# Kernel optimization log

Measured on AMD Instinct MI355X. Metric: run time of the kernel, lower is better.

## Reference

```python
import jax, jax.numpy as jnp
import numpy as np

D_MODEL = 1024
NUM_HEADS = 16
HEAD_DIM = D_MODEL // NUM_HEADS
B, S = 2, 2048


def setup_inputs() -> dict:
    key = jax.random.key(0)
    ks = jax.random.split(key, 10)
    sc = 1.0 / np.sqrt(D_MODEL)
    return {
        "x": jax.random.normal(ks[0], (B, S, D_MODEL), jnp.float32),
        "y": jax.random.normal(ks[1], (B, S, D_MODEL), jnp.float32),
        "Wkv": jax.random.normal(ks[2], (D_MODEL, 2 * D_MODEL), jnp.float32) * sc,
        "bkv": jax.random.normal(ks[3], (2 * D_MODEL,), jnp.float32) * 0.01,
        "Wq": jax.random.normal(ks[4], (D_MODEL, D_MODEL), jnp.float32) * sc,
        "bq": jax.random.normal(ks[5], (D_MODEL,), jnp.float32) * 0.01,
        "Wo": jax.random.normal(ks[6], (D_MODEL, D_MODEL), jnp.float32) * sc,
        "bo": jax.random.normal(ks[7], (D_MODEL,), jnp.float32) * 0.01,
    }


def reference(x, y, Wkv, bkv, Wq, bq, Wo, bo):
    b, s, d = x.shape
    # projections: kv from x (keys/values come from encoder side), q from y
    kv = x @ Wkv + bkv                      # [B, S, 2*d_model]
    q = y @ Wq + bq                         # [B, S, d_model]
    kv = kv.reshape(b, s, NUM_HEADS, 2 * HEAD_DIM).transpose(0, 2, 1, 3)  # [B,H,S,2*hd]
    q = q.reshape(b, s, NUM_HEADS, HEAD_DIM).transpose(0, 2, 1, 3)        # [B,H,S,hd]
    k, v = jnp.split(kv, 2, axis=-1)        # each [B,H,S,hd]
    scaled = jnp.einsum("bhqd,bhkd->bhqk", q, k) / np.sqrt(HEAD_DIM)      # [B,H,S,S]
    attention = jax.nn.softmax(scaled, axis=-1)
    values = jnp.einsum("bhqk,bhkd->bhqd", attention, v)                  # [B,H,S,hd]
    values = values.transpose(0, 2, 1, 3).reshape(b, s, d)                # [B,S,d_model]
    return values @ Wo + bo
```

## Files before the change

### kernel.cpp

```cpp
#include <hip/hip_runtime.h>
#include <hip/hip_bf16.h>

typedef __attribute__((ext_vector_type(8))) short short8;
typedef __attribute__((ext_vector_type(4))) short short4v;
typedef __attribute__((ext_vector_type(4))) float f32x4;
typedef __attribute__((ext_vector_type(16))) float f32x16;

#define B_  2
#define S_  2048
#define H_  16
#define HD_ 64
#define D_  1024
#define QSCALE 0.18033688f

__device__ __forceinline__ short f2bs(float f) {
  union { float f; unsigned u; } c; c.f = f;
  unsigned u = c.u;
  u += 0x7fffu + ((u >> 16) & 1u);
  return (short)(u >> 16);
}

__device__ __forceinline__ unsigned pack_bf16(float a, float b) {
  __hip_bfloat162 h = __float22bfloat162_rn(float2{a, b});
  return *reinterpret_cast<unsigned*>(&h);
}

__device__ __forceinline__ float fexp2(float x) {
#if __has_builtin(__builtin_amdgcn_exp2f)
  return __builtin_amdgcn_exp2f(x);
#else
  return exp2f(x);
#endif
}

__device__ __forceinline__ float frcp(float x) {
#if __has_builtin(__builtin_amdgcn_rcpf)
  return __builtin_amdgcn_rcpf(x);
#else
  return 1.0f / x;
#endif
}

#define GL2LDS(gp, lp) __builtin_amdgcn_global_load_lds( \
    (const __attribute__((address_space(1))) unsigned int*)(gp), \
    (__attribute__((address_space(3))) unsigned int*)(lp), 16, 0, 0)

#define WAITCNT4  asm volatile("s_waitcnt vmcnt(4)" ::: "memory")
#define WAITCNT8  asm volatile("s_waitcnt vmcnt(8)" ::: "memory")
#define WAITCNT0  asm volatile("s_waitcnt vmcnt(0)" ::: "memory")
#define BARRIER_PIN do { __builtin_amdgcn_s_barrier(); __builtin_amdgcn_sched_barrier(0); } while (0)

__global__ __launch_bounds__(256)
void prep_kernel(const float* __restrict__ x, const float* __restrict__ y,
                 short* __restrict__ xb, short* __restrict__ yb,
                 const float* __restrict__ Wkv, short* __restrict__ Wkvt,
                 const float* __restrict__ Wq, short* __restrict__ Wqt,
                 const float* __restrict__ Wo, short* __restrict__ Wot) {
  __shared__ float tile[64][65];
  int bx = blockIdx.x;
  if (bx < 8192) {
    int i = bx * 256 + threadIdx.x;
    const float4* src; short4v* dst; int j;
    if (i < (1 << 20)) { src = (const float4*)x; dst = (short4v*)xb; j = i; }
    else               { src = (const float4*)y; dst = (short4v*)yb; j = i - (1 << 20); }
    float4 f = src[j];
    short4v o;
    o.x = f2bs(f.x); o.y = f2bs(f.y); o.z = f2bs(f.z); o.w = f2bs(f.w);
    dst[j] = o;
    return;
  }
  bx -= 8192;
  const float* in; short* out; int C, c0, r0;
  if (bx < 512)      { in = Wkv; out = Wkvt; C = 2048; c0 = (bx & 31) * 64; r0 = (bx >> 5) * 64; }
  else if (bx < 768) { bx -= 512; in = Wq; out = Wqt; C = 1024; c0 = (bx & 15) * 64; r0 = (bx >> 4) * 64; }
  else               { bx -= 768; in = Wo; out = Wot; C = 1024; c0 = (bx & 15) * 64; r0 = (bx >> 4) * 64; }
  const int tx = threadIdx.x & 63, ty = threadIdx.x >> 6;
#pragma unroll
  for (int i = 0; i < 16; ++i) {
    int r = ty + i * 4;
    tile[r][tx] = in[(size_t)(r0 + r) * C + c0 + tx];
  }
  __syncthreads();
#pragma unroll
  for (int i = 0; i < 16; ++i) {
    int r = ty + i * 4;
    out[(size_t)(c0 + r) * 1024 + r0 + tx] = f2bs(tile[tx][r]);
  }
}

template <int MODE>
__device__ __forceinline__ void gemm_body(const short* __restrict__ A, const short* __restrict__ Bt,
                                          const float* __restrict__ bias,
                                          void* __restrict__ out0, void* __restrict__ out1,
                                          int m0, int n0, int K, short* smem) {
  short* As_ = smem;
  short* Bs_ = smem + 12288;
  const int tid = threadIdx.x;
  const int w = tid >> 6, lane = tid & 63;
  const int q15 = lane & 15, quad = lane >> 4;
  const int wm = (w >> 1) * 64, wn = (w & 1) * 64;

  f32x4 acc[4][4];
#pragma unroll
  for (int i = 0; i < 4; ++i)
#pragma unroll
    for (int j = 0; j < 4; ++j) acc[i][j] = f32x4{0.f, 0.f, 0.f, 0.f};

  const int srow = w * 16 + (lane >> 2);
  const int gch  = (lane & 3) ^ ((lane >> 3) & 3);
  const short* Ag = A + (size_t)(m0 + srow) * K + gch * 8;
  const short* Bg = Bt + (size_t)(n0 + srow) * K + gch * 8;
  const int lof = srow * 32 + (lane & 3) * 8;

#define STAGE_AB(t, buf) do { \
    const short* a2 = Ag + (size_t)(t) * 32; \
    const short* b2 = Bg + (size_t)(t) * 32; \
    short* ad = As_ + (buf) * 4096 + lof; \
    short* bd = Bs_ + (buf) * 4096 + lof; \
    GL2LDS(a2,                  ad); \
    GL2LDS(a2 + (size_t)64 * K, ad + 2048); \
    GL2LDS(b2,                  bd); \
    GL2LDS(b2 + (size_t)64 * K, bd + 2048); \
  } while (0)

  const int NT = K >> 5;
  STAGE_AB(0, 0);
  STAGE_AB(1, 1);
  int cb = 0, ib = 2;
  for (int kt = 0; kt < NT; ++kt) {
    if (kt < NT - 1) WAITCNT4; else WAITCNT0;
    BARRIER_PIN;
    if (kt + 2 < NT) STAGE_AB(kt + 2, ib);
    const short* Ac = As_ + cb * 4096;
    const short* Bc = Bs_ + cb * 4096;
    short8 af[4], bf[4];
#pragma unroll
    for (int mi = 0; mi < 4; ++mi) {
      int rr = wm + mi * 16 + q15;
      af[mi] = *(const short8*)(Ac + rr * 32 + ((quad ^ ((rr >> 1) & 3)) * 8));
    }
#pragma unroll
    for (int ni = 0; ni < 4; ++ni) {
      int rr = wn + ni * 16 + q15;
      bf[ni] = *(const short8*)(Bc + rr * 32 + ((quad ^ ((rr >> 1) & 3)) * 8));
    }
#pragma unroll
    for (int mi = 0; mi < 4; ++mi)
#pragma unroll
      for (int ni = 0; ni < 4; ++ni)
        acc[mi][ni] = __builtin_amdgcn_mfma_f32_16x16x32_bf16(af[mi], bf[ni], acc[mi][ni], 0, 0, 0);
    cb = (cb == 2) ? 0 : cb + 1;
    ib = (ib == 2) ? 0 : ib + 1;
  }
#undef STAGE_AB
  __syncthreads();

  if constexpr (MODE == 0) {
#pragma unroll
    for (int mi = 0; mi < 4; ++mi)
#pragma unroll
      for (int ni = 0; ni < 4; ++ni) {
        const int n = n0 + wn + ni * 16 + q15;
        const float bn = bias[n];
#pragma unroll
        for (int r = 0; r < 4; ++r) {
          const int m = m0 + wm + mi * 16 + quad * 4 + r;
          int b = m >> 11, s = m & 2047, hh = n >> 6, d = n & 63;
          ((short*)out0)[((size_t)((b * H_ + hh) * S_ + s) << 6) + d] = f2bs((acc[mi][ni][r] + bn) * QSCALE);
        }
      }
  } else {
    const int hh = n0 >> 7;
    const int bb = m0 >> 11;
    const size_t bh = (size_t)(bb * H_ + hh);
    const int s0 = m0 & 2047;
    if ((w & 1) == 0) {
#pragma unroll
      for (int mi = 0; mi < 4; ++mi)
#pragma unroll
        for (int ni = 0; ni < 4; ++ni) {
          const float bn = bias[n0 + ni * 16 + q15];
#pragma unroll
          for (int r = 0; r < 4; ++r) {
            const int s = s0 + wm + mi * 16 + quad * 4 + r;
            ((short*)out0)[((bh * S_ + s) << 6) + ni * 16 + q15] = f2bs(acc[mi][ni][r] + bn);
          }
        }
    } else {
      short* VT = smem;
#pragma unroll
      for (int mi = 0; mi < 4; ++mi)
#pragma unroll
        for (int ni = 0; ni < 4; ++ni) {
          const int d = ni * 16 + q15;
          const float bn = bias[n0 + 64 + ni * 16 + q15];
#pragma unroll
          for (int t = 0; t < 2; ++t) {
            const int chunk = (wm >> 1) + mi * 8 + quad * 2 + t;
            unsigned pk = pack_bf16(acc[mi][ni][2 * t] + bn, acc[mi][ni][2 * t + 1] + bn);
            *reinterpret_cast<unsigned*>(VT + d * 128 + ((chunk ^ (d & 15)) * 2)) = pk;
          }
        }
    }
    __syncthreads();
    {
      short* VT = smem;
      const int d = tid >> 2, t4 = tid & 3;
      unsigned vals[16];
#pragma unroll
      for (int c = 0; c < 16; ++c) {
        int chunk = t4 * 16 + c;
        vals[c] = *reinterpret_cast<unsigned*>(VT + d * 128 + ((chunk ^ (d & 15)) * 2));
      }
      uint4* dst = (uint4*)((short*)out1 + ((bh * HD_ + d) << 11) + s0 + t4 * 32);
      dst[0] = uint4{vals[0], vals[1], vals[4],  vals[5]};
      dst[1] = uint4{vals[2], vals[3], vals[6],  vals[7]};
      dst[2] = uint4{vals[8], vals[9], vals[12], vals[13]};
      dst[3] = uint4{vals[10], vals[11], vals[14], vals[15]};
    }
  }
}

__global__ __launch_bounds__(256)
void proj_kernel(const short* __restrict__ xb, const short* __restrict__ Wkvt,
                 const float* __restrict__ bkv, short* __restrict__ Kb, short* __restrict__ Vtb,
                 const short* __restrict__ yb, const short* __restrict__ Wqt,
                 const float* __restrict__ bq, short* __restrict__ Qb) {
  __shared__ __align__(16) short smem[24576];
  int bx = blockIdx.x;
  bx = (bx & 7) * 96 + (bx >> 3);
  if (bx < 512)
    gemm_body<1>(xb, Wkvt, bkv, Kb, Vtb, (bx >> 4) * 128, (bx & 15) * 128, 1024, smem);
  else {
    bx -= 512;
    gemm_body<0>(yb, Wqt, bq, Qb, nullptr, (bx >> 3) * 128, (bx & 7) * 128, 1024, smem);
  }
}

__global__ __launch_bounds__(256)
void gemm_o_kernel(const short* __restrict__ A, const short* __restrict__ Bt,
                   const float* __restrict__ bias, float* __restrict__ out) {
  __shared__ __align__(16) short lds[16384];
  const int tid = threadIdx.x;
  const int w = tid >> 6, lane = tid & 63;
  const int q15 = lane & 15, quad = lane >> 4;
  const int m0 = blockIdx.y * 64, n0 = blockIdx.x * 64;
  const int wm = (w >> 1) * 32, wn = (w & 1) * 32;
  const int xw = q15 & 7;

  f32x4 acc[2][2];
#pragma unroll
  for (int i = 0; i < 2; ++i)
#pragma unroll
    for (int j = 0; j < 2; ++j) acc[i][j] = f32x4{0.f, 0.f, 0.f, 0.f};

  const int srow = w * 8 + (lane >> 3);
  const int gch  = (lane & 7) ^ (srow & 7);
  const int loff = w * 512 + lane * 8;
  const short* Ag = A + (size_t)(m0 + srow) * 1024 + gch * 8;
  const short* Bg = Bt + (size_t)(n0 + srow) * 1024 + gch * 8;

  GL2LDS(Ag,             lds + loff);
  GL2LDS(Ag + 32 * 1024, lds + loff + 2048);
  GL2LDS(Bg,             lds + 8192 + loff);
  GL2LDS(Bg + 32 * 1024, lds + 8192 + loff + 2048);

  for (int kt = 0; kt < 16; ++kt) {
    __syncthreads();
    const short* Ac = lds + ((kt & 1) ? 4096 : 0);
    const short* Bc = lds + 8192 + ((kt & 1) ? 4096 : 0);
    if (kt < 15) {
      const short* a2 = Ag + (kt + 1) * 64;
      const short* b2 = Bg + (kt + 1) * 64;
      short* ad = lds + ((kt & 1) ? 0 : 4096) + loff;
      short* bd = lds + 8192 + ((kt & 1) ? 0 : 4096) + loff;
      GL2LDS(a2,             ad);
      GL2LDS(a2 + 32 * 1024, ad + 2048);
      GL2LDS(b2,             bd);
      GL2LDS(b2 + 32 * 1024, bd + 2048);
    }
    short8 af[2][2], bf[2][2];
#pragma unroll
    for (int mi = 0; mi < 2; ++mi)
#pragma unroll
      for (int kk = 0; kk < 2; ++kk)
        af[mi][kk] = *(const short8*)(Ac + (wm + mi * 16 + q15) * 64 + (((kk * 4 + quad) ^ xw) * 8));
#pragma unroll
    for (int ni = 0; ni < 2; ++ni)
#pragma unroll
      for (int kk = 0; kk < 2; ++kk)
        bf[ni][kk] = *(const short8*)(Bc + (wn + ni * 16 + q15) * 64 + (((kk * 4 + quad) ^ xw) * 8));
#pragma unroll
    for (int mi = 0; mi < 2; ++mi)
#pragma unroll
      for (int ni = 0; ni < 2; ++ni)
#pragma unroll
        for (int kk = 0; kk < 2; ++kk)
          acc[mi][ni] = __builtin_amdgcn_mfma_f32_16x16x32_bf16(af[mi][kk], bf[ni][kk], acc[mi][ni], 0, 0, 0);
  }

#pragma unroll
  for (int mi = 0; mi < 2; ++mi)
#pragma unroll
    for (int ni = 0; ni < 2; ++ni) {
      const int n = n0 + wn + ni * 16 + q15;
      const float bn = bias[n];
#pragma unroll
      for (int r = 0; r < 4; ++r) {
        const int m = m0 + wm + mi * 16 + quad * 4 + r;
        out[(size_t)m * 1024 + n] = acc[mi][ni][r] + bn;
      }
    }
}

__global__ __launch_bounds__(256, 2)
void attn_kernel(const short* __restrict__ Q, const short* __restrict__ K,
                 const short* __restrict__ Vt, short* __restrict__ Out) {
  __shared__ __align__(16) short lds[32768];
  short* QP = lds + 24576;
  const int tid = threadIdx.x;
  const int w = tid >> 6, lane = tid & 63;
  const int l31 = lane & 31, h5 = lane >> 5;
  const int rsw = l31 & 7;
  const int bx = blockIdx.x;
  const int xcd = bx & 7, slot = bx >> 3;
  const int pp = xcd * 4 + (slot >> 4);
  const int qt = slot & 15;
  const int h = pp & 15, b = pp >> 4;
  const size_t bh = (size_t)(b * H_ + h);
  const short* Qg = Q + bh * (S_ * HD_) + qt * (128 * HD_);
  const short* Kg = K + bh * (S_ * HD_);
  const short* Vg = Vt + bh * (HD_ * S_);

  const int srow = tid >> 3;
  const int gch  = (tid & 7) ^ (srow & 7);
  const int loff = tid * 8;

  const short* kg = Kg + srow * 64 + gch * 8;
  const short* vg = Vg + (size_t)srow * S_ + gch * 8;

#define STAGE_KV(t, buf) do { \
    const short* k2 = kg + (size_t)(t) * 4096; \
    const short* v2 = vg + (size_t)(t) * 64; \
    short* kd = lds + (buf) * 4096 + loff; \
    short* vd = lds + 12288 + (buf) * 4096 + loff; \
    GL2LDS(k2,                   kd); \
    GL2LDS(k2 + 2048,            kd + 2048); \
    GL2LDS(v2,                   vd); \
    GL2LDS(v2 + (size_t)32 * S_, vd + 2048); \
  } while (0)

  {
    const short* qg = Qg + srow * 64 + gch * 8;
#pragma unroll
    for (int t = 0; t < 4; ++t) GL2LDS(qg + t * 2048, QP + loff + t * 2048);
  }
  STAGE_KV(0, 0);
  STAGE_KV(1, 1);
  WAITCNT8;
  BARRIER_PIN;

  short8 aq[4];
#pragma unroll
  for (int kk = 0; kk < 4; ++kk)
    aq[kk] = *(const short8*)(QP + (w * 32 + l31) * 64 + (((kk * 2 + h5) ^ rsw) * 8));

  f32x16 oacc[2];
#pragma unroll
  for (int i = 0; i < 16; ++i) { oacc[0][i] = 0.f; oacc[1][i] = 0.f; }
  float lsum = 0.f;
  f32x16 z16;
#pragma unroll
  for (int i = 0; i < 16; ++i) z16[i] = 0.f;

  int cb = 0, ib = 2;
  for (int kt = 0; kt < 32; ++kt) {
    if (kt < 31) WAITCNT4; else WAITCNT0;
    BARRIER_PIN;
    if (kt + 2 < 32) STAGE_KV(kt + 2, ib);
    const short* Kc = lds + cb * 4096;
    const short* Vc = lds + 12288 + cb * 4096;

    f32x16 sacc[2];
    __builtin_amdgcn_s_setprio(1);
#pragma unroll
    for (int sb = 0; sb < 2; ++sb) {
      const short* kr = Kc + (sb * 32 + l31) * 64;
      short8 k0 = *(const short8*)(kr + (((0 + h5) ^ rsw) * 8));
      short8 k1 = *(const short8*)(kr + (((2 + h5) ^ rsw) * 8));
      short8 k2 = *(const short8*)(kr + (((4 + h5) ^ rsw) * 8));
      short8 k3 = *(const short8*)(kr + (((6 + h5) ^ rsw) * 8));
      f32x16 s = __builtin_amdgcn_mfma_f32_32x32x16_bf16(k0, aq[0], z16, 0, 0, 0);
      s = __builtin_amdgcn_mfma_f32_32x32x16_bf16(k1, aq[1], s, 0, 0, 0);
      s = __builtin_amdgcn_mfma_f32_32x32x16_bf16(k2, aq[2], s, 0, 0, 0);
      s = __builtin_amdgcn_mfma_f32_32x32x16_bf16(k3, aq[3], s, 0, 0, 0);
      sacc[sb] = s;
    }
    __builtin_amdgcn_s_setprio(0);

    short8 ap[4];
#pragma unroll
    for (int sb = 0; sb < 2; ++sb) {
      float e[16];
#pragma unroll
      for (int i = 0; i < 16; ++i) e[i] = fexp2(sacc[sb][i]);
      lsum += (((e[0] + e[1]) + (e[2] + e[3])) + ((e[4] + e[5]) + (e[6] + e[7])))
            + (((e[8] + e[9]) + (e[10] + e[11])) + ((e[12] + e[13]) + (e[14] + e[15])));
      union { unsigned u[4]; short8 s8; } lo, hi;
      lo.u[0] = pack_bf16(e[0], e[1]);   lo.u[1] = pack_bf16(e[2], e[3]);
      lo.u[2] = pack_bf16(e[4], e[5]);   lo.u[3] = pack_bf16(e[6], e[7]);
      hi.u[0] = pack_bf16(e[8], e[9]);   hi.u[1] = pack_bf16(e[10], e[11]);
      hi.u[2] = pack_bf16(e[12], e[13]); hi.u[3] = pack_bf16(e[14], e[15]);
      ap[sb * 2 + 0] = lo.s8;
      ap[sb * 2 + 1] = hi.s8;
    }

    __builtin_amdgcn_s_setprio(1);
#pragma unroll
    for (int db = 0; db < 2; ++db) {
      const short* vr = Vc + (db * 32 + l31) * 64;
      short8 v0 = *(const short8*)(vr + (((0 + h5) ^ rsw) * 8));
      short8 v1 = *(const short8*)(vr + (((2 + h5) ^ rsw) * 8));
      short8 v2 = *(const short8*)(vr + (((4 + h5) ^ rsw) * 8));
      short8 v3 = *(const short8*)(vr + (((6 + h5) ^ rsw) * 8));
      f32x16 o = oacc[db];
      o = __builtin_amdgcn_mfma_f32_32x32x16_bf16(ap[0], v0, o, 0, 0, 0);
      o = __builtin_amdgcn_mfma_f32_32x32x16_bf16(ap[1], v1, o, 0, 0, 0);
      o = __builtin_amdgcn_mfma_f32_32x32x16_bf16(ap[2], v2, o, 0, 0, 0);
      o = __builtin_amdgcn_mfma_f32_32x32x16_bf16(ap[3], v3, o, 0, 0, 0);
      oacc[db] = o;
    }
    __builtin_amdgcn_s_setprio(0);
    cb = (cb == 2) ? 0 : cb + 1;
    ib = (ib == 2) ? 0 : ib + 1;
  }
#undef STAGE_KV

  float lt = lsum + __shfl_xor(lsum, 32);
  float inv[16];
#pragma unroll
  for (int r = 0; r < 16; ++r)
    inv[r] = frcp(__shfl(lt, (r & 3) + 8 * (r >> 2) + 4 * h5, 64));
#pragma unroll
  for (int db = 0; db < 2; ++db) {
    const int col = h * HD_ + db * 32 + l31;
#pragma unroll
    for (int r = 0; r < 16; ++r) {
      const int m = b * S_ + qt * 128 + w * 32 + (r & 3) + 8 * (r >> 2) + 4 * h5;
      Out[(size_t)m * D_ + col] = f2bs(oacc[db][r] * inv[r]);
    }
  }
}

extern "C" void kernel_launch(void* const* d_in, const int* in_sizes, int n_in,
                              void* d_out, int out_size, void* d_ws, size_t ws_size,
                              hipStream_t stream) {
  const float* x   = (const float*)d_in[0];
  const float* y   = (const float*)d_in[1];
  const float* Wkv = (const float*)d_in[2];
  const float* bkv = (const float*)d_in[3];
  const float* Wq  = (const float*)d_in[4];
  const float* bq  = (const float*)d_in[5];
  const float* Wo  = (const float*)d_in[6];
  const float* bo  = (const float*)d_in[7];
  float* out = (float*)d_out;

  short* xb   = (short*)d_ws;
  short* yb   = xb + (4 << 20);
  short* Wkvt = yb + (4 << 20);
  short* Wqt  = Wkvt + (2 << 20);
  short* Wot  = Wqt + (1 << 20);
  short* Kb   = Wot + (1 << 20);
  short* Vtb  = Kb + (4 << 20);
  short* Qb   = Vtb + (4 << 20);
  short* AOb  = Qb + (4 << 20);

  prep_kernel<<<9216, 256, 0, stream>>>(x, y, xb, yb, Wkv, Wkvt, Wq, Wqt, Wo, Wot);
  proj_kernel<<<768, 256, 0, stream>>>(xb, Wkvt, bkv, Kb, Vtb, yb, Wqt, bq, Qb);
  attn_kernel<<<512, 256, 0, stream>>>(Qb, Kb, Vtb, AOb);
  gemm_o_kernel<<<dim3(16, 64), 256, 0, stream>>>(AOb, Wot, bo, out);
}
```

Baseline: 192.8 us.

## Software-pipeline attention loop: overlap QK of tile t with PV of tile t-1

Restructures the attention inner loop so each step computes QK^T for the current K tile and PV for the previous tile's probabilities, with the softmax/exp of the current tile done after the MFMAs. The goal is to let exp and pack work overlap with matrix-core work instead of serialising QK, softmax and PV within one tile. V tiles get a fourth LDS buffer (LDS grows from 64KB to 72KB) because V lives one step longer. This adds a prologue and epilogue, doubles the registers held for probabilities, and the larger LDS footprint may affect occupancy at two blocks per CU.

```diff
diff --git a/kernel.cpp b/kernel.cpp
--- a/kernel.cpp
+++ b/kernel.cpp
@@ -46,7 +46,6 @@
     (__attribute__((address_space(3))) unsigned int*)(lp), 16, 0, 0)
 
 #define WAITCNT4  asm volatile("s_waitcnt vmcnt(4)" ::: "memory")
-#define WAITCNT8  asm volatile("s_waitcnt vmcnt(8)" ::: "memory")
 #define WAITCNT0  asm volatile("s_waitcnt vmcnt(0)" ::: "memory")
 #define BARRIER_PIN do { __builtin_amdgcn_s_barrier(); __builtin_amdgcn_sched_barrier(0); } while (0)
 
@@ -316,8 +315,8 @@
 __global__ __launch_bounds__(256, 2)
 void attn_kernel(const short* __restrict__ Q, const short* __restrict__ K,
                  const short* __restrict__ Vt, short* __restrict__ Out) {
-  __shared__ __align__(16) short lds[32768];
-  short* QP = lds + 24576;
+  __shared__ __align__(16) short lds[36864];
+  short* QP = lds + 28672;
   const int tid = threadIdx.x;
   const int w = tid >> 6, lane = tid & 63;
   const int l31 = lane & 31, h5 = lane >> 5;
@@ -339,25 +338,102 @@
   const short* kg = Kg + srow * 64 + gch * 8;
   const short* vg = Vg + (size_t)srow * S_ + gch * 8;
 
-#define STAGE_KV(t, buf) do { \
+#define STAGE_KV(t, kb, vb) do { \
     const short* k2 = kg + (size_t)(t) * 4096; \
     const short* v2 = vg + (size_t)(t) * 64; \
-    short* kd = lds + (buf) * 4096 + loff; \
-    short* vd = lds + 12288 + (buf) * 4096 + loff; \
+    short* kd = lds + (kb) * 4096 + loff; \
+    short* vd = lds + 12288 + (vb) * 4096 + loff; \
     GL2LDS(k2,                   kd); \
     GL2LDS(k2 + 2048,            kd + 2048); \
     GL2LDS(v2,                   vd); \
     GL2LDS(v2 + (size_t)32 * S_, vd + 2048); \
   } while (0)
 
+#define QK_CLUSTER(Kc, S0, S1) do { \
+    const short* kr0 = (Kc) + l31 * 64; \
+    const short* kr1 = (Kc) + (32 + l31) * 64; \
+    short8 k0 = *(const short8*)(kr0 + (((0 + h5) ^ rsw) * 8)); \
+    short8 k1 = *(const short8*)(kr0 + (((2 + h5) ^ rsw) * 8)); \
+    short8 k2 = *(const short8*)(kr0 + (((4 + h5) ^ rsw) * 8)); \
+    short8 k3 = *(const short8*)(kr0 + (((6 + h5) ^ rsw) * 8)); \
+    short8 m0 = *(const short8*)(kr1 + (((0 + h5) ^ rsw) * 8)); \
+    short8 m1 = *(const short8*)(kr1 + (((2 + h5) ^ rsw) * 8)); \
+    short8 m2 = *(const short8*)(kr1 + (((4 + h5) ^ rsw) * 8)); \
+    short8 m3 = *(const short8*)(kr1 + (((6 + h5) ^ rsw) * 8)); \
+    S0 = __builtin_amdgcn_mfma_f32_32x32x16_bf16(k0, aq[0], z16, 0, 0, 0); \
+    S0 = __builtin_amdgcn_mfma_f32_32x32x16_bf16(k1, aq[1], S0, 0, 0, 0); \
+    S0 = __builtin_amdgcn_mfma_f32_32x32x16_bf16(k2, aq[2], S0, 0, 0, 0); \
+    S0 = __builtin_amdgcn_mfma_f32_32x32x16_bf16(k3, aq[3], S0, 0, 0, 0); \
+    S1 = __builtin_amdgcn_mfma_f32_32x32x16_bf16(m0, aq[0], z16, 0, 0, 0); \
+    S1 = __builtin_amdgcn_mfma_f32_32x32x16_bf16(m1, aq[1], S1, 0, 0, 0); \
+    S1 = __builtin_amdgcn_mfma_f32_32x32x16_bf16(m2, aq[2], S1, 0, 0, 0); \
+    S1 = __builtin_amdgcn_mfma_f32_32x32x16_bf16(m3, aq[3], S1, 0, 0, 0); \
+  } while (0)
+
+#define PV_CLUSTER(Vp, AP) do { \
+    const short* vr0 = (Vp) + l31 * 64; \
+    const short* vr1 = (Vp) + (32 + l31) * 64; \
+    short8 v0 = *(const short8*)(vr0 + (((0 + h5) ^ rsw) * 8)); \
+    short8 v1 = *(const short8*)(vr0 + (((2 + h5) ^ rsw) * 8)); \
+    short8 v2 = *(const short8*)(vr0 + (((4 + h5) ^ rsw) * 8)); \
+    short8 v3 = *(const short8*)(vr0 + (((6 + h5) ^ rsw) * 8)); \
+    short8 u0 = *(const short8*)(vr1 + (((0 + h5) ^ rsw) * 8)); \
+    short8 u1 = *(const short8*)(vr1 + (((2 + h5) ^ rsw) * 8)); \
+    short8 u2 = *(const short8*)(vr1 + (((4 + h5) ^ rsw) * 8)); \
+    short8 u3 = *(const short8*)(vr1 + (((6 + h5) ^ rsw) * 8)); \
+    oacc[0] = __builtin_amdgcn_mfma_f32_32x32x16_bf16(AP[0], v0, oacc[0], 0, 0, 0); \
+    oacc[0] = __builtin_amdgcn_mfma_f32_32x32x16_bf16(AP[1], v1, oacc[0], 0, 0, 0); \
+    oacc[0] = __builtin_amdgcn_mfma_f32_32x32x16_bf16(AP[2], v2, oacc[0], 0, 0, 0); \
+    oacc[0] = __builtin_amdgcn_mfma_f32_32x32x16_bf16(AP[3], v3, oacc[0], 0, 0, 0); \
+    oacc[1] = __builtin_amdgcn_mfma_f32_32x32x16_bf16(AP[0], u0, oacc[1], 0, 0, 0); \
+    oacc[1] = __builtin_amdgcn_mfma_f32_32x32x16_bf16(AP[1], u1, oacc[1], 0, 0, 0); \
+    oacc[1] = __builtin_amdgcn_mfma_f32_32x32x16_bf16(AP[2], u2, oacc[1], 0, 0, 0); \
+    oacc[1] = __builtin_amdgcn_mfma_f32_32x32x16_bf16(AP[3], u3, oacc[1], 0, 0, 0); \
+  } while (0)
+
+#define SOFTMAX(S0, S1, AP) do { \
+    float e[16]; \
+    union { unsigned u[4]; short8 s8; } p0, p1; \
+    _Pragma("unroll") for (int i = 0; i < 16; ++i) e[i] = fexp2(S0[i]); \
+    lsum += (((e[0] + e[1]) + (e[2] + e[3])) + ((e[4] + e[5]) + (e[6] + e[7]))) \
+          + (((e[8] + e[9]) + (e[10] + e[11])) + ((e[12] + e[13]) + (e[14] + e[15]))); \
+    p0.u[0] = pack_bf16(e[0], e[1]);   p0.u[1] = pack_bf16(e[2], e[3]); \
+    p0.u[2] = pack_bf16(e[4], e[5]);   p0.u[3] = pack_bf16(e[6], e[7]); \
+    p1.u[0] = pack_bf16(e[8], e[9]);   p1.u[1] = pack_bf16(e[10], e[11]); \
+    p1.u[2] = pack_bf16(e[12], e[13]); p1.u[3] = pack_bf16(e[14], e[15]); \
+    AP[0] = p0.s8; AP[1] = p1.s8; \
+    _Pragma("unroll") for (int i = 0; i < 16; ++i) e[i] = fexp2(S1[i]); \
+    lsum += (((e[0] + e[1]) + (e[2] + e[3])) + ((e[4] + e[5]) + (e[6] + e[7]))) \
+          + (((e[8] + e[9]) + (e[10] + e[11])) + ((e[12] + e[13]) + (e[14] + e[15]))); \
+    p0.u[0] = pack_bf16(e[0], e[1]);   p0.u[1] = pack_bf16(e[2], e[3]); \
+    p0.u[2] = pack_bf16(e[4], e[5]);   p0.u[3] = pack_bf16(e[6], e[7]); \
+    p1.u[0] = pack_bf16(e[8], e[9]);   p1.u[1] = pack_bf16(e[10], e[11]); \
+    p1.u[2] = pack_bf16(e[12], e[13]); p1.u[3] = pack_bf16(e[14], e[15]); \
+    AP[2] = p0.s8; AP[3] = p1.s8; \
+  } while (0)
+
+#define ATTN_STEP(kt, APIN, APOUT) do { \
+    if ((kt) < 31) WAITCNT4; else WAITCNT0; \
+    BARRIER_PIN; \
+    if ((kt) + 2 < 32) STAGE_KV((kt) + 2, ((kt) + 2) % 3, ((kt) + 2) & 3); \
+    const short* Kc = lds + ((kt) % 3) * 4096; \
+    const short* Vp = lds + 12288 + (((kt) + 3) & 3) * 4096; \
+    f32x16 s0, s1; \
+    __builtin_amdgcn_s_setprio(1); \
+    QK_CLUSTER(Kc, s0, s1); \
+    PV_CLUSTER(Vp, APIN); \
+    __builtin_amdgcn_s_setprio(0); \
+    SOFTMAX(s0, s1, APOUT); \
+  } while (0)
+
   {
     const short* qg = Qg + srow * 64 + gch * 8;
 #pragma unroll
     for (int t = 0; t < 4; ++t) GL2LDS(qg + t * 2048, QP + loff + t * 2048);
   }
-  STAGE_KV(0, 0);
-  STAGE_KV(1, 1);
-  WAITCNT8;
+  STAGE_KV(0, 0, 0);
+  STAGE_KV(1, 1, 1);
+  WAITCNT4;
   BARRIER_PIN;
 
   short8 aq[4];
@@ -373,67 +449,31 @@
 #pragma unroll
   for (int i = 0; i < 16; ++i) z16[i] = 0.f;
 
-  int cb = 0, ib = 2;
-  for (int kt = 0; kt < 32; ++kt) {
-    if (kt < 31) WAITCNT4; else WAITCNT0;
-    BARRIER_PIN;
-    if (kt + 2 < 32) STAGE_KV(kt + 2, ib);
-    const short* Kc = lds + cb * 4096;
-    const short* Vc = lds + 12288 + cb * 4096;
-
-    f32x16 sacc[2];
+  short8 apA[4], apB[4];
+  {
+    STAGE_KV(2, 2, 2);
+    const short* Kc = lds;
+    f32x16 s0, s1;
     __builtin_amdgcn_s_setprio(1);
-#pragma unroll
-    for (int sb = 0; sb < 2; ++sb) {
-      const short* kr = Kc + (sb * 32 + l31) * 64;
-      short8 k0 = *(const short8*)(kr + (((0 + h5) ^ rsw) * 8));
-      short8 k1 = *(const short8*)(kr + (((2 + h5) ^ rsw) * 8));
-      short8 k2 = *(const short8*)(kr + (((4 + h5) ^ rsw) * 8));
-      short8 k3 = *(const short8*)(kr + (((6 + h5) ^ rsw) * 8));
-      f32x16 s = __builtin_amdgcn_mfma_f32_32x32x16_bf16(k0, aq[0], z16, 0, 0, 0);
-      s = __builtin_amdgcn_mfma_f32_32x32x16_bf16(k1, aq[1], s, 0, 0, 0);
-      s = __builtin_amdgcn_mfma_f32_32x32x16_bf16(k2, aq[2], s, 0, 0, 0);
-      s = __builtin_amdgcn_mfma_f32_32x32x16_bf16(k3, aq[3], s, 0, 0, 0);
-      sacc[sb] = s;
-    }
+    QK_CLUSTER(Kc, s0, s1);
     __builtin_amdgcn_s_setprio(0);
-
-    short8 ap[4];
-#pragma unroll
-    for (int sb = 0; sb < 2; ++sb) {
-      float e[16];
-#pragma unroll
-      for (int i = 0; i < 16; ++i) e[i] = fexp2(sacc[sb][i]);
-      lsum += (((e[0] + e[1]) + (e[2] + e[3])) + ((e[4] + e[5]) + (e[6] + e[7])))
-            + (((e[8] + e[9]) + (e[10] + e[11])) + ((e[12] + e[13]) + (e[14] + e[15])));
-      union { unsigned u[4]; short8 s8; } lo, hi;
-      lo.u[0] = pack_bf16(e[0], e[1]);   lo.u[1] = pack_bf16(e[2], e[3]);
-      lo.u[2] = pack_bf16(e[4], e[5]);   lo.u[3] = pack_bf16(e[6], e[7]);
-      hi.u[0] = pack_bf16(e[8], e[9]);   hi.u[1] = pack_bf16(e[10], e[11]);
-      hi.u[2] = pack_bf16(e[12], e[13]); hi.u[3] = pack_bf16(e[14], e[15]);
-      ap[sb * 2 + 0] = lo.s8;
-      ap[sb * 2 + 1] = hi.s8;
-    }
-
+    SOFTMAX(s0, s1, apA);
+  }
+  for (int kt = 1; kt < 31; kt += 2) {
+    ATTN_STEP(kt,     apA, apB);
+    ATTN_STEP(kt + 1, apB, apA);
+  }
+  ATTN_STEP(31, apA, apB);
+  {
+    const short* Vp = lds + 12288 + 3 * 4096;
     __builtin_amdgcn_s_setprio(1);
-#pragma unroll
-    for (int db = 0; db < 2; ++db) {
-      const short* vr = Vc + (db * 32 + l31) * 64;
-      short8 v0 = *(const short8*)(vr + (((0 + h5) ^ rsw) * 8));
-      short8 v1 = *(const short8*)(vr + (((2 + h5) ^ rsw) * 8));
-      short8 v2 = *(const short8*)(vr + (((4 + h5) ^ rsw) * 8));
-      short8 v3 = *(const short8*)(vr + (((6 + h5) ^ rsw) * 8));
-      f32x16 o = oacc[db];
-      o = __builtin_amdgcn_mfma_f32_32x32x16_bf16(ap[0], v0, o, 0, 0, 0);
-      o = __builtin_amdgcn_mfma_f32_32x32x16_bf16(ap[1], v1, o, 0, 0, 0);
-      o = __builtin_amdgcn_mfma_f32_32x32x16_bf16(ap[2], v2, o, 0, 0, 0);
-      o = __builtin_amdgcn_mfma_f32_32x32x16_bf16(ap[3], v3, o, 0, 0, 0);
-      oacc[db] = o;
-    }
+    PV_CLUSTER(Vp, apB);
     __builtin_amdgcn_s_setprio(0);
-    cb = (cb == 2) ? 0 : cb + 1;
-    ib = (ib == 2) ? 0 : ib + 1;
-  }
+  }
+#undef ATTN_STEP
+#undef SOFTMAX
+#undef PV_CLUSTER
+#undef QK_CLUSTER
 #undef STAGE_KV
 
   float lt = lsum + __shfl_xor(lsum, 32);
```

New measurement: 197.4 us. +2.4%, slower.

## Triple-buffer output GEMM; widen attention blocks to 512 threads with double buffering

Applied to the files above, without the earlier changes.

The output-projection GEMM moves from a two-buffer loop with a full barrier to a three-stage ring that prefetches two tiles ahead and waits on vmcnt, so load latency is better hidden. The attention kernel now runs 512 threads per block covering 256 query rows, so each staged K/V tile is shared by twice as many waves and global traffic for K/V drops. Its K/V pipeline falls back to simple double buffering with __syncthreads, and the grid is halved to 256 blocks. The risk is lower occupancy and less latency hiding in attention, plus less parallelism across CUs.

```diff
diff --git a/kernel.cpp b/kernel.cpp
--- a/kernel.cpp
+++ b/kernel.cpp
@@ -46,7 +46,6 @@
     (__attribute__((address_space(3))) unsigned int*)(lp), 16, 0, 0)
 
 #define WAITCNT4  asm volatile("s_waitcnt vmcnt(4)" ::: "memory")
-#define WAITCNT8  asm volatile("s_waitcnt vmcnt(8)" ::: "memory")
 #define WAITCNT0  asm volatile("s_waitcnt vmcnt(0)" ::: "memory")
 #define BARRIER_PIN do { __builtin_amdgcn_s_barrier(); __builtin_amdgcn_sched_barrier(0); } while (0)
 
@@ -240,7 +239,7 @@
 __global__ __launch_bounds__(256)
 void gemm_o_kernel(const short* __restrict__ A, const short* __restrict__ Bt,
                    const float* __restrict__ bias, float* __restrict__ out) {
-  __shared__ __align__(16) short lds[16384];
+  __shared__ __align__(16) short lds[24576];
   const int tid = threadIdx.x;
   const int w = tid >> 6, lane = tid & 63;
   const int q15 = lane & 15, quad = lane >> 4;
@@ -260,25 +259,26 @@
   const short* Ag = A + (size_t)(m0 + srow) * 1024 + gch * 8;
   const short* Bg = Bt + (size_t)(n0 + srow) * 1024 + gch * 8;
 
-  GL2LDS(Ag,             lds + loff);
-  GL2LDS(Ag + 32 * 1024, lds + loff + 2048);
-  GL2LDS(Bg,             lds + 8192 + loff);
-  GL2LDS(Bg + 32 * 1024, lds + 8192 + loff + 2048);
-
+#define STAGE_O(t, buf) do { \
+    const short* a2 = Ag + (size_t)(t) * 64; \
+    const short* b2 = Bg + (size_t)(t) * 64; \
+    short* ad = lds + (buf) * 4096 + loff; \
+    short* bd = lds + 12288 + (buf) * 4096 + loff; \
+    GL2LDS(a2,             ad); \
+    GL2LDS(a2 + 32 * 1024, ad + 2048); \
+    GL2LDS(b2,             bd); \
+    GL2LDS(b2 + 32 * 1024, bd + 2048); \
+  } while (0)
+
+  STAGE_O(0, 0);
+  STAGE_O(1, 1);
+  int cb = 0, ib = 2;
   for (int kt = 0; kt < 16; ++kt) {
-    __syncthreads();
-    const short* Ac = lds + ((kt & 1) ? 4096 : 0);
-    const short* Bc = lds + 8192 + ((kt & 1) ? 4096 : 0);
-    if (kt < 15) {
-      const short* a2 = Ag + (kt + 1) * 64;
-      const short* b2 = Bg + (kt + 1) * 64;
-      short* ad = lds + ((kt & 1) ? 0 : 4096) + loff;
-      short* bd = lds + 8192 + ((kt & 1) ? 0 : 4096) + loff;
-      GL2LDS(a2,             ad);
-      GL2LDS(a2 + 32 * 1024, ad + 2048);
-      GL2LDS(b2,             bd);
-      GL2LDS(b2 + 32 * 1024, bd + 2048);
-    }
+    if (kt < 15) WAITCNT4; else WAITCNT0;
+    BARRIER_PIN;
+    if (kt + 2 < 16) STAGE_O(kt + 2, ib);
+    const short* Ac = lds + cb * 4096;
+    const short* Bc = lds + 12288 + cb * 4096;
     short8 af[2][2], bf[2][2];
 #pragma unroll
     for (int mi = 0; mi < 2; ++mi)
@@ -297,7 +297,10 @@
 #pragma unroll
         for (int kk = 0; kk < 2; ++kk)
           acc[mi][ni] = __builtin_amdgcn_mfma_f32_16x16x32_bf16(af[mi][kk], bf[ni][kk], acc[mi][ni], 0, 0, 0);
-  }
+    cb = (cb == 2) ? 0 : cb + 1;
+    ib = (ib == 2) ? 0 : ib + 1;
+  }
+#undef STAGE_O
 
 #pragma unroll
   for (int mi = 0; mi < 2; ++mi)
@@ -313,52 +316,39 @@
     }
 }
 
-__global__ __launch_bounds__(256, 2)
+__global__ __launch_bounds__(512, 2)
 void attn_kernel(const short* __restrict__ Q, const short* __restrict__ K,
                  const short* __restrict__ Vt, short* __restrict__ Out) {
   __shared__ __align__(16) short lds[32768];
-  short* QP = lds + 24576;
+  short* QP = lds + 16384;
   const int tid = threadIdx.x;
   const int w = tid >> 6, lane = tid & 63;
   const int l31 = lane & 31, h5 = lane >> 5;
   const int rsw = l31 & 7;
   const int bx = blockIdx.x;
   const int xcd = bx & 7, slot = bx >> 3;
-  const int pp = xcd * 4 + (slot >> 4);
-  const int qt = slot & 15;
+  const int pp = xcd * 4 + (slot >> 3);
+  const int qt = slot & 7;
   const int h = pp & 15, b = pp >> 4;
   const size_t bh = (size_t)(b * H_ + h);
-  const short* Qg = Q + bh * (S_ * HD_) + qt * (128 * HD_);
+  const short* Qg = Q + bh * (S_ * HD_) + qt * (256 * HD_);
   const short* Kg = K + bh * (S_ * HD_);
   const short* Vg = Vt + bh * (HD_ * S_);
 
-  const int srow = tid >> 3;
-  const int gch  = (tid & 7) ^ (srow & 7);
-  const int loff = tid * 8;
-
+  const int srow = w * 8 + (lane >> 3);
+  const int gch  = (lane & 7) ^ (srow & 7);
+  const int loff = w * 512 + lane * 8;
+
+  {
+    const short* qg = Qg + srow * 64 + gch * 8;
+#pragma unroll
+    for (int t = 0; t < 4; ++t) GL2LDS(qg + t * 4096, QP + loff + t * 4096);
+  }
   const short* kg = Kg + srow * 64 + gch * 8;
   const short* vg = Vg + (size_t)srow * S_ + gch * 8;
-
-#define STAGE_KV(t, buf) do { \
-    const short* k2 = kg + (size_t)(t) * 4096; \
-    const short* v2 = vg + (size_t)(t) * 64; \
-    short* kd = lds + (buf) * 4096 + loff; \
-    short* vd = lds + 12288 + (buf) * 4096 + loff; \
-    GL2LDS(k2,                   kd); \
-    GL2LDS(k2 + 2048,            kd + 2048); \
-    GL2LDS(v2,                   vd); \
-    GL2LDS(v2 + (size_t)32 * S_, vd + 2048); \
-  } while (0)
-
-  {
-    const short* qg = Qg + srow * 64 + gch * 8;
-#pragma unroll
-    for (int t = 0; t < 4; ++t) GL2LDS(qg + t * 2048, QP + loff + t * 2048);
-  }
-  STAGE_KV(0, 0);
-  STAGE_KV(1, 1);
-  WAITCNT8;
-  BARRIER_PIN;
+  GL2LDS(kg, lds + loff);
+  GL2LDS(vg, lds + 8192 + loff);
+  __syncthreads();
 
   short8 aq[4];
 #pragma unroll
@@ -373,13 +363,16 @@
 #pragma unroll
   for (int i = 0; i < 16; ++i) z16[i] = 0.f;
 
-  int cb = 0, ib = 2;
   for (int kt = 0; kt < 32; ++kt) {
-    if (kt < 31) WAITCNT4; else WAITCNT0;
-    BARRIER_PIN;
-    if (kt + 2 < 32) STAGE_KV(kt + 2, ib);
-    const short* Kc = lds + cb * 4096;
-    const short* Vc = lds + 12288 + cb * 4096;
+    __syncthreads();
+    const short* Kc = lds + ((kt & 1) ? 4096 : 0);
+    const short* Vc = lds + 8192 + ((kt & 1) ? 4096 : 0);
+    if (kt < 31) {
+      const short* k2 = kg + (kt + 1) * 4096;
+      const short* v2 = vg + (kt + 1) * 64;
+      GL2LDS(k2, lds + ((kt & 1) ? 0 : 4096) + loff);
+      GL2LDS(v2, lds + 8192 + ((kt & 1) ? 0 : 4096) + loff);
+    }
 
     f32x16 sacc[2];
     __builtin_amdgcn_s_setprio(1);
@@ -431,10 +424,7 @@
       oacc[db] = o;
     }
     __builtin_amdgcn_s_setprio(0);
-    cb = (cb == 2) ? 0 : cb + 1;
-    ib = (ib == 2) ? 0 : ib + 1;
-  }
-#undef STAGE_KV
+  }
 
   float lt = lsum + __shfl_xor(lsum, 32);
   float inv[16];
@@ -446,7 +436,7 @@
     const int col = h * HD_ + db * 32 + l31;
 #pragma unroll
     for (int r = 0; r < 16; ++r) {
-      const int m = b * S_ + qt * 128 + w * 32 + (r & 3) + 8 * (r >> 2) + 4 * h5;
+      const int m = b * S_ + qt * 256 + w * 32 + (r & 3) + 8 * (r >> 2) + 4 * h5;
       Out[(size_t)m * D_ + col] = f2bs(oacc[db][r] * inv[r]);
     }
   }
@@ -477,6 +467,6 @@
 
   prep_kernel<<<9216, 256, 0, stream>>>(x, y, xb, yb, Wkv, Wkvt, Wq, Wqt, Wo, Wot);
   proj_kernel<<<768, 256, 0, stream>>>(xb, Wkvt, bkv, Kb, Vtb, yb, Wqt, bq, Qb);
-  attn_kernel<<<512, 256, 0, stream>>>(Qb, Kb, Vtb, AOb);
+  attn_kernel<<<256, 512, 0, stream>>>(Qb, Kb, Vtb, AOb);
   gemm_o_kernel<<<dim3(16, 64), 256, 0, stream>>>(AOb, Wot, bo, out);
 }
```

After: 194.9 us. Within noise of the previous version (+1.1%).
